# Kernel optimization log

Hardware: AMD Instinct MI355X
Metric: run time of the kernel (lower is better)

## Reference

```python
import jax, jax.numpy as jnp
import numpy as np

BXYZ = 4
L = 1_000_000
C = 64
KERNEL = 2
N_BATCH = 4
GRID = 1024


def setup_inputs() -> dict:
    key = jax.random.key(0)
    k1, k2, k3 = jax.random.split(key, 3)
    in_feats = jax.random.normal(k1, (L, C), dtype=jnp.float32)
    b = jax.random.randint(k2, (L, 1), 0, N_BATCH, dtype=jnp.int32)
    xyz = jax.random.randint(k3, (L, 3), 0, GRID, dtype=jnp.int32)
    in_coords = jnp.concatenate([b, xyz], axis=1)  # [L, 4] = (batch, x, y, z)
    return {"in_feats": in_feats, "in_coords": in_coords, "kernel_size": KERNEL}


def _encode(coords):
    # mixed-radix encoding: (((b)*X + x)*Y + y)*Z + z with per-dim extents
    min_c = coords.min(axis=0)            # [4]
    c = coords - min_c
    max_c = c.max(axis=0) + 1             # [4] radices
    enc = c[:, 0]
    for i in range(1, BXYZ):
        enc = enc * max_c[i] + c[:, i]
    return enc, min_c, max_c


def _decode(enc, min_c, max_c):
    cols = []
    for idx in range(BXYZ - 1, -1, -1):
        rem = enc % max_c[idx]
        cols.append(min_c[idx] + rem)
        enc = (enc - rem) // max_c[idx]
    return jnp.stack(cols[::-1], axis=1)  # [L*, 4]


def reference(in_feats, in_coords, kernel_size):
    # downsample spatial coords (keep batch column)
    coords = in_coords.at[:, 1:].set(in_coords[:, 1:] // kernel_size)
    enc, min_c, max_c = _encode(coords)
    n = enc.shape[0]
    # jit-compatible unique padded to n (torch returns only the unique rows;
    # here trailing padded rows carry -inf feats / fill coords)
    uniq, inv = jnp.unique(enc, return_inverse=True, size=n, fill_value=0)
    out_feats = jnp.full((n, in_feats.shape[1]), -jnp.inf, dtype=in_feats.dtype)
    out_feats = out_feats.at[inv].max(in_feats)  # scatter-amax, include_self=False
    out_coords = _decode(uniq, min_c, max_c)
    return out_feats, out_coords
```

## Files before the change

### kernel.cpp

```cpp
#include <hip/hip_runtime.h>
#include <climits>
#include <cstdint>
#include <cstddef>
#include <math.h>


static constexpr int kNumGroups = 1 << 21;
static constexpr int kNumWords  = 1 << 24;
static constexpr size_t kBitmapBytes = (size_t)kNumWords * 4;

typedef float f32x4 __attribute__((ext_vector_type(4)));

#define GS(i, n) for (int i = blockIdx.x * blockDim.x + threadIdx.x; i < (n); i += gridDim.x * blockDim.x)

__global__ void k_init(int* wsi) {
    int t = threadIdx.x;
    if (t < 4) wsi[t] = INT_MAX;
    else if (t < 8) wsi[t] = INT_MIN;
}

__global__ void k_minmax(const int4* __restrict__ coords, const int* __restrict__ ksp,
                         int L, int* wsi) {
    int ks = *ksp;
    int mn[4] = {INT_MAX, INT_MAX, INT_MAX, INT_MAX};
    int mx[4] = {INT_MIN, INT_MIN, INT_MIN, INT_MIN};
    GS(i, L) {
        int4 c = coords[i];
        int v0 = c.x, v1 = c.y / ks, v2 = c.z / ks, v3 = c.w / ks;
        mn[0] = min(mn[0], v0); mx[0] = max(mx[0], v0);
        mn[1] = min(mn[1], v1); mx[1] = max(mx[1], v1);
        mn[2] = min(mn[2], v2); mx[2] = max(mx[2], v2);
        mn[3] = min(mn[3], v3); mx[3] = max(mx[3], v3);
    }
    #pragma unroll
    for (int off = 32; off; off >>= 1) {
        #pragma unroll
        for (int k = 0; k < 4; ++k) {
            mn[k] = min(mn[k], __shfl_down(mn[k], off));
            mx[k] = max(mx[k], __shfl_down(mx[k], off));
        }
    }
    __shared__ int smn[16], smx[16];
    int wave = threadIdx.x >> 6, lane = threadIdx.x & 63;
    if (lane == 0) {
        #pragma unroll
        for (int k = 0; k < 4; ++k) { smn[wave * 4 + k] = mn[k]; smx[wave * 4 + k] = mx[k]; }
    }
    __syncthreads();
    if (threadIdx.x < 4) {
        int k = threadIdx.x;
        int a = min(min(smn[k], smn[4 + k]), min(smn[8 + k], smn[12 + k]));
        int b = max(max(smx[k], smx[4 + k]), max(smx[8 + k], smx[12 + k]));
        atomicMin(&wsi[k], a);
        atomicMax(&wsi[4 + k], b);
    }
}

__global__ void k_encode(const int4* __restrict__ coords, const int* __restrict__ ksp, int L,
                         const int* __restrict__ wsi, unsigned* __restrict__ enc,
                         unsigned* __restrict__ bitmap) {
    int ks = *ksp;
    int mn0 = wsi[0], mn1 = wsi[1], mn2 = wsi[2], mn3 = wsi[3];
    unsigned m1 = (unsigned)(wsi[5] - mn1 + 1);
    unsigned m2 = (unsigned)(wsi[6] - mn2 + 1);
    unsigned m3 = (unsigned)(wsi[7] - mn3 + 1);
    GS(i, L) {
        int4 c = coords[i];
        unsigned c0 = (unsigned)(c.x - mn0);
        unsigned c1 = (unsigned)(c.y / ks - mn1);
        unsigned c2 = (unsigned)(c.z / ks - mn2);
        unsigned c3 = (unsigned)(c.w / ks - mn3);
        unsigned e = ((c0 * m1 + c1) * m2 + c2) * m3 + c3;
        unsigned bit = 1u << (e & 31u);
        unsigned old = atomicOr(&bitmap[e >> 5], bit);
        enc[i] = e | ((old & bit) ? 0x80000000u : 0u);
    }
}

__global__ void k_groupcnt(const unsigned* __restrict__ bitmap, unsigned* __restrict__ ctaSums) {
    int g = blockIdx.x * blockDim.x + threadIdx.x;
    const uint4* p = (const uint4*)(bitmap + ((size_t)g << 3));
    uint4 a = p[0], b = p[1];
    unsigned s = __popc(a.x) + __popc(a.y) + __popc(a.z) + __popc(a.w)
               + __popc(b.x) + __popc(b.y) + __popc(b.z) + __popc(b.w);
    __shared__ unsigned sm[256];
    sm[threadIdx.x] = s;
    __syncthreads();
    for (int off = 128; off; off >>= 1) {
        if (threadIdx.x < off) sm[threadIdx.x] += sm[threadIdx.x + off];
        __syncthreads();
    }
    if (threadIdx.x == 0) ctaSums[blockIdx.x] = sm[0];
}

__global__ void k_scan_cta(const unsigned* __restrict__ ctaSums, unsigned* __restrict__ ctaPref,
                           int* wsi) {
    int t = threadIdx.x;
    unsigned v[8]; unsigned ts = 0;
    #pragma unroll
    for (int j = 0; j < 8; ++j) { v[j] = ctaSums[t * 8 + j]; ts += v[j]; }
    __shared__ unsigned sm[1024];
    sm[t] = ts;
    __syncthreads();
    for (int off = 1; off < 1024; off <<= 1) {
        unsigned add = (t >= off) ? sm[t - off] : 0u;
        __syncthreads();
        sm[t] += add;
        __syncthreads();
    }
    unsigned run = sm[t] - ts;
    #pragma unroll
    for (int j = 0; j < 8; ++j) { ctaPref[t * 8 + j] = run; run += v[j]; }
    if (t == 1023) wsi[14] = (int)sm[1023];
}

__global__ void k_gpref_coords(const unsigned* __restrict__ bitmap,
                               const unsigned* __restrict__ ctaPref,
                               const int* __restrict__ wsi,
                               unsigned* __restrict__ gpref,
                               float* __restrict__ outc, int L) {
    int g = blockIdx.x * blockDim.x + threadIdx.x;
    const uint4* p = (const uint4*)(bitmap + ((size_t)g << 3));
    uint4 a = p[0], b4 = p[1];
    unsigned s = __popc(a.x) + __popc(a.y) + __popc(a.z) + __popc(a.w)
               + __popc(b4.x) + __popc(b4.y) + __popc(b4.z) + __popc(b4.w);
    __shared__ unsigned sm[256];
    int t = threadIdx.x;
    sm[t] = s;
    __syncthreads();
    for (int off = 1; off < 256; off <<= 1) {
        unsigned add = (t >= off) ? sm[t - off] : 0u;
        __syncthreads();
        sm[t] += add;
        __syncthreads();
    }
    unsigned rank = ctaPref[blockIdx.x] + sm[t] - s;
    gpref[g] = rank;

    int mn0 = wsi[0], mn1 = wsi[1], mn2 = wsi[2], mn3 = wsi[3];
    unsigned m1 = (unsigned)(wsi[5] - mn1 + 1);
    unsigned m2 = (unsigned)(wsi[6] - mn2 + 1);
    unsigned m3 = (unsigned)(wsi[7] - mn3 + 1);
    unsigned wv[8] = {a.x, a.y, a.z, a.w, b4.x, b4.y, b4.z, b4.w};
    #pragma unroll
    for (int j = 0; j < 8; ++j) {
        unsigned bits = wv[j];
        unsigned wbase = (((unsigned)g << 3) + (unsigned)j) << 5;
        while (bits) {
            unsigned b = (unsigned)__ffs(bits) - 1u;
            bits &= bits - 1u;
            unsigned code = wbase | b;
            unsigned c3 = code % m3; code /= m3;
            unsigned c2 = code % m2; code /= m2;
            unsigned c1 = code % m1; code /= m1;
            float4 o = make_float4((float)(mn0 + (int)code), (float)(mn1 + (int)c1),
                                   (float)(mn2 + (int)c2), (float)(mn3 + (int)c3));
            ((float4*)outc)[rank] = o;
            rank++;
        }
    }
    int K = wsi[14];
    float4 o = make_float4((float)mn0, (float)mn1, (float)mn2, (float)mn3);
    int total = gridDim.x * blockDim.x;
    for (int r = K + g; r < L; r += total)
        ((float4*)outc)[r] = o;
}

__global__ void k_rank(const unsigned* __restrict__ enc, const unsigned* __restrict__ bitmap,
                       const unsigned* __restrict__ gpref, int L,
                       unsigned* __restrict__ inv, unsigned* __restrict__ srcrow) {
    int t = blockIdx.x * blockDim.x + threadIdx.x;
    int base = t * 4;
    if (base >= L) return;
    uint4 ev = *(const uint4*)(enc + base);
    unsigned es[4] = {ev.x, ev.y, ev.z, ev.w};
    #pragma unroll
    for (int j = 0; j < 4; ++j) {
        int i = base + j;
        if (i >= L) break;
        unsigned ei = es[j];
        unsigned dup = ei & 0x80000000u;
        unsigned e = ei & 0x1FFFFFFFu;
        unsigned w = e >> 5, g = w >> 3, wb = w & 7u;
        const uint4* p = (const uint4*)(bitmap + ((size_t)g << 3));
        uint4 a = p[0], b = p[1];
        unsigned r = gpref[g];
        r += (wb > 0) ? __popc(a.x) : 0u;
        r += (wb > 1) ? __popc(a.y) : 0u;
        r += (wb > 2) ? __popc(a.z) : 0u;
        r += (wb > 3) ? __popc(a.w) : 0u;
        r += (wb > 4) ? __popc(b.x) : 0u;
        r += (wb > 5) ? __popc(b.y) : 0u;
        r += (wb > 6) ? __popc(b.z) : 0u;
        unsigned word = (wb < 4) ? ((wb < 2) ? (wb == 0 ? a.x : a.y) : (wb == 2 ? a.z : a.w))
                                 : ((wb < 6) ? (wb == 4 ? b.x : b.y) : (wb == 6 ? b.z : b.w));
        r += __popc(word & ((1u << (e & 31u)) - 1u));
        inv[i] = r | dup;
        if (!dup) srcrow[r] = (unsigned)i;
    }
}

__global__ void k_gather3(const f32x4* __restrict__ feats4, const unsigned* __restrict__ srcrow,
                          const int* __restrict__ wsi, int L, f32x4* __restrict__ out4) {
    int wpb = blockDim.x >> 6;
    int gw = gridDim.x * wpb;
    int w = blockIdx.x * wpb + (threadIdx.x >> 6);
    int lane = threadIdx.x & 63;
    int sub = lane >> 4;
    int q   = lane & 15;
    int K = wsi[14];
    const int U = 8;
    const int RPI = 4 * U;
    for (int r0 = w * RPI; r0 < L; r0 += gw * RPI) {
        int r[U]; unsigned s[U];
        #pragma unroll
        for (int j = 0; j < U; ++j) {
            r[j] = r0 + j * 4 + sub;
            s[j] = (r[j] < K) ? srcrow[r[j]] : 0xFFFFFFFFu;
        }
        f32x4 v[U];
        #pragma unroll
        for (int j = 0; j < U; ++j) {
            v[j] = (s[j] != 0xFFFFFFFFu)
                     ? __builtin_nontemporal_load(&feats4[(size_t)s[j] * 16 + q])
                     : (f32x4){0.f, 0.f, 0.f, 0.f};
        }
        #pragma unroll
        for (int j = 0; j < U; ++j)
            if (r[j] < L) __builtin_nontemporal_store(v[j], &out4[(size_t)r[j] * 16 + q]);
    }
}

__global__ void k_gather3_gen(const float* __restrict__ feats, const unsigned* __restrict__ srcrow,
                              const int* __restrict__ wsi, int L, int C, float* __restrict__ out) {
    int wpb = blockDim.x >> 6;
    int gw = gridDim.x * wpb;
    int w = blockIdx.x * wpb + (threadIdx.x >> 6);
    int lane = threadIdx.x & 63;
    int K = wsi[14];
    for (int r = w; r < L; r += gw) {
        if (r < K) {
            unsigned s = srcrow[r];
            for (int cc = lane; cc < C; cc += 64)
                out[(size_t)r * C + cc] = feats[(size_t)s * C + cc];
        } else {
            for (int cc = lane; cc < C; cc += 64) out[(size_t)r * C + cc] = 0.0f;
        }
    }
}

__device__ inline void atomicMaxFloat(float* addr, float val) {
    unsigned* ua = (unsigned*)addr;
    unsigned old = *((volatile unsigned*)ua);
    while (__uint_as_float(old) < val) {
        unsigned assumed = old;
        old = atomicCAS(ua, assumed, __float_as_uint(val));
        if (old == assumed) break;
    }
}

__global__ void k_fix(const float* __restrict__ feats, const unsigned* __restrict__ inv,
                      int L, int C, float* __restrict__ out) {
    int lane = threadIdx.x & 63;
    int stride = gridDim.x * blockDim.x;
    for (int i = blockIdx.x * blockDim.x + threadIdx.x; i - lane < L; i += stride) {
        unsigned e = (i < L) ? inv[i] : 0u;
        bool multi = (e >> 31) != 0u;
        unsigned long long mask = __ballot(multi);
        while (mask) {
            int srcl = __ffsll((unsigned long long)mask) - 1;
            mask &= mask - 1ull;
            int id = __shfl(i, srcl);
            int row = __shfl((int)(e & 0x7FFFFFFFu), srcl);
            for (int cc = lane; cc < C; cc += 64)
                atomicMaxFloat(&out[(size_t)row * C + cc], feats[(size_t)id * C + cc]);
        }
    }
}

extern "C" void kernel_launch(void* const* d_in, const int* in_sizes, int n_in,
                              void* d_out, int out_size, void* d_ws, size_t ws_size,
                              hipStream_t stream) {
    const float* feats = (const float*)d_in[0];
    const int4* coords = (const int4*)d_in[1];
    const int* ksp     = (const int*)d_in[2];
    int L = in_sizes[1] / 4;
    int C = in_sizes[0] / L;

    char* ob = (char*)d_out;
    unsigned* bitmap = (unsigned*)ob;
    unsigned* gpref  = (unsigned*)(ob + kBitmapBytes);
    unsigned* enc    = gpref + kNumGroups;
    float* out_feats  = (float*)d_out;
    float* out_coords = out_feats + (size_t)L * C;

    char* wsb = (char*)d_ws;
    int* wsi = (int*)wsb;
    unsigned* ctaSums = (unsigned*)(wsb + 4096);
    unsigned* ctaPref = (unsigned*)(wsb + 4096 + 32768);
    unsigned* inv     = (unsigned*)(wsb + (1 << 20));
    unsigned* srcrow  = inv + L;

    (void)hipMemsetAsync(bitmap, 0, kBitmapBytes, stream);
    k_init<<<1, 64, 0, stream>>>(wsi);
    k_minmax<<<256, 256, 0, stream>>>(coords, ksp, L, wsi);
    k_encode<<<1024, 256, 0, stream>>>(coords, ksp, L, wsi, enc, bitmap);
    k_groupcnt<<<kNumGroups / 256, 256, 0, stream>>>(bitmap, ctaSums);
    k_scan_cta<<<1, 1024, 0, stream>>>(ctaSums, ctaPref, wsi);
    k_gpref_coords<<<kNumGroups / 256, 256, 0, stream>>>(bitmap, ctaPref, wsi, gpref, out_coords, L);
    k_rank<<<(L + 1023) / 1024, 256, 0, stream>>>(enc, bitmap, gpref, L, inv, srcrow);
    if (C == 64)
        k_gather3<<<2048, 256, 0, stream>>>((const f32x4*)feats, srcrow, wsi, L, (f32x4*)out_feats);
    else
        k_gather3_gen<<<2048, 256, 0, stream>>>(feats, srcrow, wsi, L, C, out_feats);
    k_fix<<<2048, 256, 0, stream>>>(feats, inv, L, C, out_feats);
}
```

Measured before the change: 274.0 us.

## Store per-group local prefix in 16-bit, widen bitmap groups to 16 words

Doubles the bitmap group size to 16 words and has the group-count kernel write a 16-bit local exclusive prefix per group instead of a full 32-bit global prefix. The coords and rank kernels rebuild the rank from the per-CTA prefix plus the local prefix. This cuts the number of groups and the prefix traffic. The encode and rank kernels also switch from a grid-stride loop to a fixed four-elements-per-thread mapping with strided access. In exchange, each rank lookup now reads 64 bytes of bitmap and does more popcounts, and each coords thread walks twice as many words.

```diff
diff --git a/kernel.cpp b/kernel.cpp
--- a/kernel.cpp
+++ b/kernel.cpp
@@ -5,8 +5,9 @@
 #include <math.h>
 
 
-static constexpr int kNumGroups = 1 << 21;
 static constexpr int kNumWords  = 1 << 24;
+static constexpr int kNumGroups = kNumWords / 16;
+static constexpr int kNumCtas   = kNumGroups / 256;
 static constexpr size_t kBitmapBytes = (size_t)kNumWords * 4;
 
 typedef float f32x4 __attribute__((ext_vector_type(4)));
@@ -64,66 +65,34 @@
     unsigned m1 = (unsigned)(wsi[5] - mn1 + 1);
     unsigned m2 = (unsigned)(wsi[6] - mn2 + 1);
     unsigned m3 = (unsigned)(wsi[7] - mn3 + 1);
-    GS(i, L) {
-        int4 c = coords[i];
-        unsigned c0 = (unsigned)(c.x - mn0);
-        unsigned c1 = (unsigned)(c.y / ks - mn1);
-        unsigned c2 = (unsigned)(c.z / ks - mn2);
-        unsigned c3 = (unsigned)(c.w / ks - mn3);
-        unsigned e = ((c0 * m1 + c1) * m2 + c2) * m3 + c3;
-        unsigned bit = 1u << (e & 31u);
-        unsigned old = atomicOr(&bitmap[e >> 5], bit);
-        enc[i] = e | ((old & bit) ? 0x80000000u : 0u);
-    }
-}
-
-__global__ void k_groupcnt(const unsigned* __restrict__ bitmap, unsigned* __restrict__ ctaSums) {
+    int base = blockIdx.x * (blockDim.x * 4) + threadIdx.x;
+    #pragma unroll
+    for (int j = 0; j < 4; ++j) {
+        int i = base + j * 256;
+        if (i < L) {
+            int4 c = coords[i];
+            unsigned c0 = (unsigned)(c.x - mn0);
+            unsigned c1 = (unsigned)(c.y / ks - mn1);
+            unsigned c2 = (unsigned)(c.z / ks - mn2);
+            unsigned c3 = (unsigned)(c.w / ks - mn3);
+            unsigned e = ((c0 * m1 + c1) * m2 + c2) * m3 + c3;
+            unsigned bit = 1u << (e & 31u);
+            unsigned old = atomicOr(&bitmap[e >> 5], bit);
+            enc[i] = e | ((old & bit) ? 0x80000000u : 0u);
+        }
+    }
+}
+
+__global__ void k_groupcnt(const unsigned* __restrict__ bitmap,
+                           unsigned short* __restrict__ lpref16,
+                           unsigned* __restrict__ ctaSums) {
     int g = blockIdx.x * blockDim.x + threadIdx.x;
-    const uint4* p = (const uint4*)(bitmap + ((size_t)g << 3));
-    uint4 a = p[0], b = p[1];
+    const uint4* p = (const uint4*)(bitmap + ((size_t)g << 4));
+    uint4 a = p[0], b = p[1], c = p[2], d = p[3];
     unsigned s = __popc(a.x) + __popc(a.y) + __popc(a.z) + __popc(a.w)
-               + __popc(b.x) + __popc(b.y) + __popc(b.z) + __popc(b.w);
-    __shared__ unsigned sm[256];
-    sm[threadIdx.x] = s;
-    __syncthreads();
-    for (int off = 128; off; off >>= 1) {
-        if (threadIdx.x < off) sm[threadIdx.x] += sm[threadIdx.x + off];
-        __syncthreads();
-    }
-    if (threadIdx.x == 0) ctaSums[blockIdx.x] = sm[0];
-}
-
-__global__ void k_scan_cta(const unsigned* __restrict__ ctaSums, unsigned* __restrict__ ctaPref,
-                           int* wsi) {
-    int t = threadIdx.x;
-    unsigned v[8]; unsigned ts = 0;
-    #pragma unroll
-    for (int j = 0; j < 8; ++j) { v[j] = ctaSums[t * 8 + j]; ts += v[j]; }
-    __shared__ unsigned sm[1024];
-    sm[t] = ts;
-    __syncthreads();
-    for (int off = 1; off < 1024; off <<= 1) {
-        unsigned add = (t >= off) ? sm[t - off] : 0u;
-        __syncthreads();
-        sm[t] += add;
-        __syncthreads();
-    }
-    unsigned run = sm[t] - ts;
-    #pragma unroll
-    for (int j = 0; j < 8; ++j) { ctaPref[t * 8 + j] = run; run += v[j]; }
-    if (t == 1023) wsi[14] = (int)sm[1023];
-}
-
-__global__ void k_gpref_coords(const unsigned* __restrict__ bitmap,
-                               const unsigned* __restrict__ ctaPref,
-                               const int* __restrict__ wsi,
-                               unsigned* __restrict__ gpref,
-                               float* __restrict__ outc, int L) {
-    int g = blockIdx.x * blockDim.x + threadIdx.x;
-    const uint4* p = (const uint4*)(bitmap + ((size_t)g << 3));
-    uint4 a = p[0], b4 = p[1];
-    unsigned s = __popc(a.x) + __popc(a.y) + __popc(a.z) + __popc(a.w)
-               + __popc(b4.x) + __popc(b4.y) + __popc(b4.z) + __popc(b4.w);
+               + __popc(b.x) + __popc(b.y) + __popc(b.z) + __popc(b.w)
+               + __popc(c.x) + __popc(c.y) + __popc(c.z) + __popc(c.w)
+               + __popc(d.x) + __popc(d.y) + __popc(d.z) + __popc(d.w);
     __shared__ unsigned sm[256];
     int t = threadIdx.x;
     sm[t] = s;
@@ -134,18 +103,50 @@
         sm[t] += add;
         __syncthreads();
     }
-    unsigned rank = ctaPref[blockIdx.x] + sm[t] - s;
-    gpref[g] = rank;
-
+    lpref16[g] = (unsigned short)(sm[t] - s);
+    if (t == 255) ctaSums[blockIdx.x] = sm[255];
+}
+
+__global__ void k_scan_cta(const unsigned* __restrict__ ctaSums, unsigned* __restrict__ ctaPref,
+                           int* wsi) {
+    int t = threadIdx.x;
+    unsigned v[4]; unsigned ts = 0;
+    #pragma unroll
+    for (int j = 0; j < 4; ++j) { v[j] = ctaSums[t * 4 + j]; ts += v[j]; }
+    __shared__ unsigned sm[1024];
+    sm[t] = ts;
+    __syncthreads();
+    for (int off = 1; off < 1024; off <<= 1) {
+        unsigned add = (t >= off) ? sm[t - off] : 0u;
+        __syncthreads();
+        sm[t] += add;
+        __syncthreads();
+    }
+    unsigned run = sm[t] - ts;
+    #pragma unroll
+    for (int j = 0; j < 4; ++j) { ctaPref[t * 4 + j] = run; run += v[j]; }
+    if (t == 1023) wsi[14] = (int)sm[1023];
+}
+
+__global__ void k_coords(const unsigned* __restrict__ bitmap,
+                         const unsigned short* __restrict__ lpref16,
+                         const unsigned* __restrict__ ctaPref,
+                         const int* __restrict__ wsi,
+                         float* __restrict__ outc, int L) {
+    int g = blockIdx.x * blockDim.x + threadIdx.x;
+    const uint4* p = (const uint4*)(bitmap + ((size_t)g << 4));
+    uint4 a = p[0], b4 = p[1], c4 = p[2], d4 = p[3];
+    unsigned rank = ctaPref[blockIdx.x] + lpref16[g];
     int mn0 = wsi[0], mn1 = wsi[1], mn2 = wsi[2], mn3 = wsi[3];
     unsigned m1 = (unsigned)(wsi[5] - mn1 + 1);
     unsigned m2 = (unsigned)(wsi[6] - mn2 + 1);
     unsigned m3 = (unsigned)(wsi[7] - mn3 + 1);
-    unsigned wv[8] = {a.x, a.y, a.z, a.w, b4.x, b4.y, b4.z, b4.w};
-    #pragma unroll
-    for (int j = 0; j < 8; ++j) {
+    unsigned wv[16] = {a.x, a.y, a.z, a.w, b4.x, b4.y, b4.z, b4.w,
+                       c4.x, c4.y, c4.z, c4.w, d4.x, d4.y, d4.z, d4.w};
+    #pragma unroll
+    for (int j = 0; j < 16; ++j) {
         unsigned bits = wv[j];
-        unsigned wbase = (((unsigned)g << 3) + (unsigned)j) << 5;
+        unsigned wbase = (((unsigned)g << 4) + (unsigned)j) << 5;
         while (bits) {
             unsigned b = (unsigned)__ffs(bits) - 1u;
             bits &= bits - 1u;
@@ -167,33 +168,47 @@
 }
 
 __global__ void k_rank(const unsigned* __restrict__ enc, const unsigned* __restrict__ bitmap,
-                       const unsigned* __restrict__ gpref, int L,
+                       const unsigned short* __restrict__ lpref16,
+                       const unsigned* __restrict__ ctaPref, int L,
                        unsigned* __restrict__ inv, unsigned* __restrict__ srcrow) {
-    int t = blockIdx.x * blockDim.x + threadIdx.x;
-    int base = t * 4;
-    if (base >= L) return;
-    uint4 ev = *(const uint4*)(enc + base);
-    unsigned es[4] = {ev.x, ev.y, ev.z, ev.w};
+    int base = blockIdx.x * (blockDim.x * 4) + threadIdx.x;
     #pragma unroll
     for (int j = 0; j < 4; ++j) {
-        int i = base + j;
-        if (i >= L) break;
-        unsigned ei = es[j];
+        int i = base + j * 256;
+        if (i >= L) continue;
+        unsigned ei = enc[i];
         unsigned dup = ei & 0x80000000u;
         unsigned e = ei & 0x1FFFFFFFu;
-        unsigned w = e >> 5, g = w >> 3, wb = w & 7u;
-        const uint4* p = (const uint4*)(bitmap + ((size_t)g << 3));
-        uint4 a = p[0], b = p[1];
-        unsigned r = gpref[g];
-        r += (wb > 0) ? __popc(a.x) : 0u;
-        r += (wb > 1) ? __popc(a.y) : 0u;
-        r += (wb > 2) ? __popc(a.z) : 0u;
-        r += (wb > 3) ? __popc(a.w) : 0u;
-        r += (wb > 4) ? __popc(b.x) : 0u;
-        r += (wb > 5) ? __popc(b.y) : 0u;
-        r += (wb > 6) ? __popc(b.z) : 0u;
-        unsigned word = (wb < 4) ? ((wb < 2) ? (wb == 0 ? a.x : a.y) : (wb == 2 ? a.z : a.w))
-                                 : ((wb < 6) ? (wb == 4 ? b.x : b.y) : (wb == 6 ? b.z : b.w));
+        unsigned w = e >> 5;
+        unsigned g = e >> 9;
+        unsigned wb = w & 15u;
+        const uint4* p = (const uint4*)(bitmap + ((size_t)g << 4));
+        uint4 a = p[0], b = p[1], c = p[2], d = p[3];
+        unsigned w0 = a.x, w1 = a.y, w2 = a.z, w3 = a.w;
+        unsigned w4 = b.x, w5 = b.y, w6 = b.z, w7 = b.w;
+        unsigned w8 = c.x, w9 = c.y, w10 = c.z, w11 = c.w;
+        unsigned w12 = d.x, w13 = d.y, w14 = d.z, w15 = d.w;
+        unsigned r = ctaPref[e >> 17] + (unsigned)lpref16[g];
+        r += (wb > 0)  ? __popc(w0)  : 0u;
+        r += (wb > 1)  ? __popc(w1)  : 0u;
+        r += (wb > 2)  ? __popc(w2)  : 0u;
+        r += (wb > 3)  ? __popc(w3)  : 0u;
+        r += (wb > 4)  ? __popc(w4)  : 0u;
+        r += (wb > 5)  ? __popc(w5)  : 0u;
+        r += (wb > 6)  ? __popc(w6)  : 0u;
+        r += (wb > 7)  ? __popc(w7)  : 0u;
+        r += (wb > 8)  ? __popc(w8)  : 0u;
+        r += (wb > 9)  ? __popc(w9)  : 0u;
+        r += (wb > 10) ? __popc(w10) : 0u;
+        r += (wb > 11) ? __popc(w11) : 0u;
+        r += (wb > 12) ? __popc(w12) : 0u;
+        r += (wb > 13) ? __popc(w13) : 0u;
+        r += (wb > 14) ? __popc(w14) : 0u;
+        unsigned word =
+            wb < 8 ? (wb < 4 ? (wb < 2 ? (wb == 0 ? w0 : w1) : (wb == 2 ? w2 : w3))
+                             : (wb < 6 ? (wb == 4 ? w4 : w5) : (wb == 6 ? w6 : w7)))
+                   : (wb < 12 ? (wb < 10 ? (wb == 8 ? w8 : w9) : (wb == 10 ? w10 : w11))
+                              : (wb < 14 ? (wb == 12 ? w12 : w13) : (wb == 14 ? w14 : w15)));
         r += __popc(word & ((1u << (e & 31u)) - 1u));
         inv[i] = r | dup;
         if (!dup) srcrow[r] = (unsigned)i;
@@ -289,26 +304,28 @@
 
     char* ob = (char*)d_out;
     unsigned* bitmap = (unsigned*)ob;
-    unsigned* gpref  = (unsigned*)(ob + kBitmapBytes);
-    unsigned* enc    = gpref + kNumGroups;
+    unsigned* enc    = (unsigned*)(ob + kBitmapBytes);
+    unsigned short* lpref16 = (unsigned short*)(ob + kBitmapBytes + (size_t)L * 4);
     float* out_feats  = (float*)d_out;
     float* out_coords = out_feats + (size_t)L * C;
 
     char* wsb = (char*)d_ws;
     int* wsi = (int*)wsb;
     unsigned* ctaSums = (unsigned*)(wsb + 4096);
-    unsigned* ctaPref = (unsigned*)(wsb + 4096 + 32768);
+    unsigned* ctaPref = (unsigned*)(wsb + 65536);
     unsigned* inv     = (unsigned*)(wsb + (1 << 20));
     unsigned* srcrow  = inv + L;
+
+    int pblocks = (L + 1023) / 1024;
 
     (void)hipMemsetAsync(bitmap, 0, kBitmapBytes, stream);
     k_init<<<1, 64, 0, stream>>>(wsi);
     k_minmax<<<256, 256, 0, stream>>>(coords, ksp, L, wsi);
-    k_encode<<<1024, 256, 0, stream>>>(coords, ksp, L, wsi, enc, bitmap);
-    k_groupcnt<<<kNumGroups / 256, 256, 0, stream>>>(bitmap, ctaSums);
+    k_encode<<<pblocks, 256, 0, stream>>>(coords, ksp, L, wsi, enc, bitmap);
+    k_groupcnt<<<kNumCtas, 256, 0, stream>>>(bitmap, lpref16, ctaSums);
     k_scan_cta<<<1, 1024, 0, stream>>>(ctaSums, ctaPref, wsi);
-    k_gpref_coords<<<kNumGroups / 256, 256, 0, stream>>>(bitmap, ctaPref, wsi, gpref, out_coords, L);
-    k_rank<<<(L + 1023) / 1024, 256, 0, stream>>>(enc, bitmap, gpref, L, inv, srcrow);
+    k_coords<<<kNumCtas, 256, 0, stream>>>(bitmap, lpref16, ctaPref, wsi, out_coords, L);
+    k_rank<<<pblocks, 256, 0, stream>>>(enc, bitmap, lpref16, ctaPref, L, inv, srcrow);
     if (C == 64)
         k_gather3<<<2048, 256, 0, stream>>>((const f32x4*)feats, srcrow, wsi, L, (f32x4*)out_feats);
     else
```

New measurement: 262.8 us. 1.04x faster.
